# Kernel optimization log

Hardware: AMD Instinct MI355X
Metric: run time of the kernel (lower is better)

Reference implementation:

```python
import jax, jax.numpy as jnp
import numpy as np

B, L, D, H = 2, 2048, 1024, 16
DH = D // H


def setup_inputs() -> dict:
    key = jax.random.key(0)
    ks = jax.random.split(key, 5)
    bound = 1.0 / D ** 0.5
    x = jax.random.normal(ks[0], (B, L, D), dtype=jnp.float32)
    # causal mask: 0 means masked out
    mask = jnp.tril(jnp.ones((L, L), dtype=jnp.int32))[None].repeat(B, axis=0)
    Wq = jax.random.uniform(ks[1], (D, D), jnp.float32, -bound, bound)
    Wk = jax.random.uniform(ks[2], (D, D), jnp.float32, -bound, bound)
    Wv = jax.random.uniform(ks[3], (D, D), jnp.float32, -bound, bound)
    Wo = jax.random.uniform(ks[4], (D, D), jnp.float32, -bound, bound)
    return {"x": x, "mask": mask, "Wq": Wq, "Wk": Wk, "Wv": Wv, "Wo": Wo}


def _split_heads(t):
    # (B, L, D) -> (B, H, L, DH)
    b, l, _ = t.shape
    return t.reshape(b, l, H, DH).transpose(0, 2, 1, 3)


def reference(x, mask, Wq, Wk, Wv, Wo):
    # projections: torch Linear does x @ W.T with W:(out,in)
    q = _split_heads(x @ Wq.T)  # (B,H,L,DH)
    k = _split_heads(x @ Wk.T)
    v = _split_heads(x @ Wv.T)
    scores = jnp.einsum('bhqd,bhkd->bhqk', q, k) / jnp.sqrt(jnp.float32(DH))
    m = mask[:, None, :, :]  # (B,1,L,L)
    scores = jnp.where(m == 0, jnp.float32(-jnp.inf), scores)
    attn = jax.nn.softmax(scores, axis=-1)
    out = jnp.einsum('bhqk,bhkd->bhqd', attn, v)  # (B,H,L,DH)
    out = out.transpose(0, 2, 1, 3).reshape(x.shape[0], x.shape[1], D)
    return out @ Wo.T
```

## Files before the change

kernel.cpp:

```cpp
#include <hip/hip_runtime.h>
#include <stdint.h>


typedef unsigned short u16;
typedef __attribute__((ext_vector_type(8))) short short8;
typedef __attribute__((ext_vector_type(4))) float f32x4;
typedef __attribute__((ext_vector_type(4))) unsigned int uint4v;

#define NEG_BIG (-1e30f)
#define QSCALE 0.18033688011112042f

__device__ __forceinline__ f32x4 mfma16(short8 a, short8 b, f32x4 c) {
    return __builtin_amdgcn_mfma_f32_16x16x32_bf16(a, b, c, 0, 0, 0);
}

__device__ __forceinline__ u16 f2bf(float f) {
    uint32_t u = __float_as_uint(f);
    u += 0x7fffu + ((u >> 16) & 1u);
    return (u16)(u >> 16);
}

__device__ __forceinline__ float bf2f(u16 v) {
    return __uint_as_float((uint32_t)v << 16);
}

#if __has_builtin(__builtin_amdgcn_cvt_pk_bf16_f32)
__device__ __forceinline__ unsigned int f2bf_pk(float a, float b) {
    return __builtin_bit_cast(unsigned int, __builtin_amdgcn_cvt_pk_bf16_f32(a, b));
}
#else
__device__ __forceinline__ unsigned int f2bf_pk(float a, float b) {
    return (unsigned int)f2bf(a) | ((unsigned int)f2bf(b) << 16);
}
#endif

__device__ __forceinline__ void load_lds_16B(const u16* g, u16* lds_base) {
    __builtin_amdgcn_global_load_lds(
        (__attribute__((address_space(1))) void*)(uintptr_t)(const void*)g,
        (__attribute__((address_space(3))) void*)lds_base,
        16, 0, 0);
}

__global__ __launch_bounds__(256) void cvt_kernel(
    const float* __restrict__ x, const float* __restrict__ wq, const float* __restrict__ wk,
    const float* __restrict__ wv, const float* __restrict__ wo, u16* __restrict__ dst)
{
    const int gid = blockIdx.x * 256 + threadIdx.x;
    const float* src; size_t off;
    if (gid < 524288)      { src = x;  off = (size_t)gid * 8; }
    else if (gid < 655360) { src = wq; off = (size_t)(gid - 524288) * 8; }
    else if (gid < 786432) { src = wk; off = (size_t)(gid - 655360) * 8; }
    else if (gid < 917504) { src = wv; off = (size_t)(gid - 786432) * 8; }
    else                   { src = wo; off = (size_t)(gid - 917504) * 8; }
    float4 a = *(const float4*)(src + off);
    float4 b = *(const float4*)(src + off + 4);
    uint4v u = { f2bf_pk(a.x, a.y), f2bf_pk(a.z, a.w),
                 f2bf_pk(b.x, b.y), f2bf_pk(b.z, b.w) };
    *(uint4v*)(dst + (size_t)gid * 8) = u;
}

__device__ __forceinline__ void gemm_bt_128x128_bk64(
    const u16* __restrict__ A, const u16* __restrict__ Bw,
    u16* at, u16* bt, int m0, int n0, f32x4 acc[4][4])
{
    const int tid  = threadIdx.x;
    const int w    = tid >> 6, lane = tid & 63;
    const int quad = lane >> 4, l15 = lane & 15;
    const int wm   = (w >> 1) * 64, wn = (w & 1) * 64;
    const int srow = lane >> 3;
    const int sch  = lane & 7;

    for (int k0 = 0; k0 < 1024; k0 += 64) {
#pragma unroll
        for (int c = 0; c < 4; ++c) {
            int row = w * 32 + c * 8 + srow;
            int g   = sch ^ (row & 7);
            load_lds_16B(A  + (size_t)(m0 + row) * 1024 + k0 + g * 8, at + (w * 32 + c * 8) * 64);
            load_lds_16B(Bw + (size_t)(n0 + row) * 1024 + k0 + g * 8, bt + (w * 32 + c * 8) * 64);
        }
        __syncthreads();
#pragma unroll
        for (int ks = 0; ks < 2; ++ks) {
            short8 af[4], bf[4];
#pragma unroll
            for (int rf = 0; rf < 4; ++rf) {
                int ra = wm + rf * 16 + l15, pa = (ks * 4 + quad) ^ (ra & 7);
                af[rf] = *(const short8*)(at + ra * 64 + pa * 8);
                int rb = wn + rf * 16 + l15, pb = (ks * 4 + quad) ^ (rb & 7);
                bf[rf] = *(const short8*)(bt + rb * 64 + pb * 8);
            }
#pragma unroll
            for (int rf = 0; rf < 4; ++rf)
#pragma unroll
                for (int cf = 0; cf < 4; ++cf)
                    acc[rf][cf] = mfma16(af[rf], bf[cf], acc[rf][cf]);
        }
        __syncthreads();
    }
}

__global__ __launch_bounds__(256, 3) void qkv_gemm(
    const u16* __restrict__ xb, const u16* __restrict__ Wq, const u16* __restrict__ Wk,
    const u16* __restrict__ Wv, u16* __restrict__ qbuf, u16* __restrict__ kbuf,
    u16* __restrict__ vtbuf)
{
    __shared__ __align__(16) u16 at[128 * 64];
    __shared__ __align__(16) u16 bt[128 * 64];
    const int m0  = blockIdx.x * 128;
    const int by  = blockIdx.y;
    const int sel = by >> 3;
    const int n0  = (by & 7) * 128;
    const u16* Wsel = sel == 0 ? Wq : (sel == 1 ? Wk : Wv);

    f32x4 acc[4][4];
    const f32x4 z = {0.f, 0.f, 0.f, 0.f};
#pragma unroll
    for (int i = 0; i < 4; ++i)
#pragma unroll
        for (int j = 0; j < 4; ++j) acc[i][j] = z;

    gemm_bt_128x128_bk64(xb, Wsel, at, bt, m0, n0, acc);

    const int tid  = threadIdx.x, w = tid >> 6, lane = tid & 63;
    const int quad = lane >> 4, l15 = lane & 15;
    const int wm   = (w >> 1) * 64, wn = (w & 1) * 64;

    if (sel < 2) {
        u16* dst = sel == 0 ? qbuf : kbuf;
        const float scl = sel == 0 ? QSCALE : 1.0f;
#pragma unroll
        for (int rf = 0; rf < 4; ++rf)
#pragma unroll
            for (int cf = 0; cf < 4; ++cf) {
                int n = n0 + wn + cf * 16 + l15;
                int h = n >> 6, dh = n & 63;
#pragma unroll
                for (int r = 0; r < 4; ++r) {
                    int m = m0 + wm + rf * 16 + quad * 4 + r;
                    int b = m >> 11, l = m & 2047;
                    dst[(((size_t)(b * 16 + h)) * 2048 + l) * 64 + dh] = f2bf(acc[rf][cf][r] * scl);
                }
            }
    } else {
#pragma unroll
        for (int rf = 0; rf < 4; ++rf)
#pragma unroll
            for (int cf = 0; cf < 4; ++cf) {
                int n = n0 + wn + cf * 16 + l15;
                int h = n >> 6, dh = n & 63;
                int m = m0 + wm + rf * 16 + quad * 4;
                int b = m >> 11, l = m & 2047;
                ushort4 pk;
                pk.x = f2bf(acc[rf][cf][0]);
                pk.y = f2bf(acc[rf][cf][1]);
                pk.z = f2bf(acc[rf][cf][2]);
                pk.w = f2bf(acc[rf][cf][3]);
                *(ushort4*)(vtbuf + (((size_t)(b * 16 + h)) * 64 + dh) * 2048 + l) = pk;
            }
    }
}


struct Chain {
    short8 qf[2];
    f32x4  o[4];
    float  m, l;
};

__device__ __forceinline__ void attn_visit(
    const u16* ktb, const u16* vtb, u16* pw,
    Chain& c, int k0, int qrow, bool diag, int quad, int l15)
{
    const f32x4 z = {0.f, 0.f, 0.f, 0.f};
    f32x4 st[4];
#pragma unroll
    for (int nf = 0; nf < 4; ++nf) st[nf] = z;
#pragma unroll
    for (int ks = 0; ks < 2; ++ks)
#pragma unroll
        for (int nf = 0; nf < 4; ++nf) {
            int row = nf * 16 + l15;
            int ph  = (ks * 4 + quad) ^ (row & 7);
            short8 kf = *(const short8*)(ktb + row * 64 + ph * 8);
            st[nf] = mfma16(kf, c.qf[ks], st[nf]);
        }
    if (diag) {
#pragma unroll
        for (int nf = 0; nf < 4; ++nf)
#pragma unroll
            for (int r = 0; r < 4; ++r) {
                int key = k0 + nf * 16 + quad * 4 + r;
                if (key > qrow) st[nf][r] = NEG_BIG;
            }
    }
    {
        float mx = st[0][0];
#pragma unroll
        for (int nf = 0; nf < 4; ++nf)
#pragma unroll
            for (int r = 0; r < 4; ++r) mx = fmaxf(mx, st[nf][r]);
        mx = fmaxf(mx, __shfl_xor(mx, 16));
        mx = fmaxf(mx, __shfl_xor(mx, 32));
        float mnew = fmaxf(c.m, mx);
        float alpha = exp2f(c.m - mnew);
        float sum = 0.f;
#pragma unroll
        for (int nf = 0; nf < 4; ++nf)
#pragma unroll
            for (int r = 0; r < 4; ++r) {
                float p = exp2f(st[nf][r] - mnew);
                st[nf][r] = p;
                sum += p;
            }
        sum += __shfl_xor(sum, 16);
        sum += __shfl_xor(sum, 32);
        c.l = c.l * alpha + sum;
        c.m = mnew;
#pragma unroll
        for (int df = 0; df < 4; ++df) c.o[df] *= alpha;
    }
#pragma unroll
    for (int nf = 0; nf < 4; ++nf) {
        int ph = (nf * 2 + (quad >> 1)) ^ (l15 & 7);
        uint2 pk2;
        pk2.x = f2bf_pk(st[nf][0], st[nf][1]);
        pk2.y = f2bf_pk(st[nf][2], st[nf][3]);
        *(uint2*)(pw + l15 * 64 + ph * 8 + (quad & 1) * 4) = pk2;
    }
#pragma unroll
    for (int ks2 = 0; ks2 < 2; ++ks2) {
        int phb = (ks2 * 4 + quad) ^ (l15 & 7);
        short8 pb = *(const short8*)(pw + l15 * 64 + phb * 8);
#pragma unroll
        for (int df = 0; df < 4; ++df) {
            int row = df * 16 + l15;
            int ph  = (ks2 * 4 + quad) ^ (row & 7);
            short8 vf = *(const short8*)(vtb + row * 64 + ph * 8);
            c.o[df] = mfma16(vf, pb, c.o[df]);
        }
    }
}

__global__ __launch_bounds__(256, 4) void attn_kernel(
    const u16* __restrict__ qbuf, const u16* __restrict__ kbuf,
    const u16* __restrict__ vtbuf, u16* __restrict__ attn,
    u16* __restrict__ po, float* __restrict__ pm, float* __restrict__ pl)
{
    __shared__ __align__(16) u16 kt[2][64 * 64];
    __shared__ __align__(16) u16 vt[2][64 * 64];
    __shared__ __align__(16) u16 pt[4 * 16 * 64];

    const int tid  = threadIdx.x, w = tid >> 6, lane = tid & 63;
    const int quad = lane >> 4, l15 = lane & 15;
    const int bh   = blockIdx.y;
    const int a    = blockIdx.x >> 1;
    const int role = blockIdx.x & 1;
    const int jqS  = a, jqB = 31 - a;

    const u16* qbase = qbuf  + (size_t)bh * 2048 * 64;
    const u16* kbase = kbuf  + (size_t)bh * 2048 * 64;
    const u16* vbase = vtbuf + (size_t)bh * 64 * 2048;
    u16* pw = pt + w * (16 * 64);
    const int b = bh >> 4, h = bh & 15;
    const int rowi = w * 16 + l15;

    const f32x4 z = {0.f, 0.f, 0.f, 0.f};

    auto stage = [&](int t, int buf) {
        const int k0 = t * 64;
#pragma unroll
        for (int c = 0; c < 2; ++c) {
            int row = w * 16 + c * 8 + (lane >> 3);
            int g   = (lane & 7) ^ (row & 7);
            load_lds_16B(kbase + (size_t)(k0 + row) * 64 + g * 8, kt[buf] + (w * 16 + c * 8) * 64);
            load_lds_16B(vbase + (size_t)row * 2048 + k0 + g * 8, vt[buf] + (w * 16 + c * 8) * 64);
        }
    };

    auto load_q = [&](int jq, Chain& c) {
        int qw = jq * 64 + w * 16;
#pragma unroll
        for (int ks = 0; ks < 2; ++ks)
            c.qf[ks] = *(const short8*)(qbase + (size_t)(qw + l15) * 64 + ks * 32 + quad * 8);
        c.m = NEG_BIG; c.l = 0.f;
#pragma unroll
        for (int df = 0; df < 4; ++df) c.o[df] = z;
    };

    if (role == 0) {
        Chain cS, cB;
        load_q(jqS, cS);
        load_q(jqB, cB);
        const int tS = a, tB = 15 - a;
        const int T0 = tS > tB ? tS : tB;
        stage(0, 0);
        for (int t = 0; t <= T0; ++t) {
            __syncthreads();
            if (t < T0) stage(t + 1, (t + 1) & 1);
            const u16* ktb = kt[t & 1];
            const u16* vtb = vt[t & 1];
            const int k0 = t * 64;
            if (t <= tB) attn_visit(ktb, vtb, pw, cB, k0, 0, false, quad, l15);
            if (t <= tS) attn_visit(ktb, vtb, pw, cS, k0, jqS * 64 + rowi, t == tS, quad, l15);
        }
        {
            float inv = 1.f / cS.l;
            int qrow = jqS * 64 + rowi;
            u16* obase = attn + ((size_t)(b * 2048 + qrow)) * 1024 + h * 64;
#pragma unroll
            for (int df = 0; df < 4; ++df)
#pragma unroll
                for (int r = 0; r < 4; ++r)
                    obase[df * 16 + quad * 4 + r] = f2bf(cS.o[df][r] * inv);
        }
        {
            int p = (bh * 16 + a) * 2 + 0;
            u16* ob = po + (size_t)p * 4096 + rowi * 64;
#pragma unroll
            for (int df = 0; df < 4; ++df)
#pragma unroll
                for (int r = 0; r < 4; ++r)
                    ob[df * 16 + quad * 4 + r] = f2bf(cB.o[df][r]);
            if (quad == 0) { pm[p * 64 + rowi] = cB.m; pl[p * 64 + rowi] = cB.l; }
        }
    } else {
        Chain cB;
        load_q(jqB, cB);
        const int tb = 16 - a, te = 31 - a;
        stage(tb, tb & 1);
        for (int t = tb; t <= te; ++t) {
            __syncthreads();
            if (t < te) stage(t + 1, (t + 1) & 1);
            attn_visit(kt[t & 1], vt[t & 1], pw, cB, t * 64, jqB * 64 + rowi, t == te, quad, l15);
        }
        int p = (bh * 16 + a) * 2 + 1;
        u16* ob = po + (size_t)p * 4096 + rowi * 64;
#pragma unroll
        for (int df = 0; df < 4; ++df)
#pragma unroll
            for (int r = 0; r < 4; ++r)
                ob[df * 16 + quad * 4 + r] = f2bf(cB.o[df][r]);
        if (quad == 0) { pm[p * 64 + rowi] = cB.m; pl[p * 64 + rowi] = cB.l; }
    }
}

__global__ __launch_bounds__(256) void merge_kernel(
    const u16* __restrict__ po, const float* __restrict__ pm, const float* __restrict__ pl,
    u16* __restrict__ attn)
{
    const int u   = blockIdx.x;
    const int bh  = u >> 4, a = u & 15;
    const int b   = bh >> 4, h = bh & 15;
    const int jqB = 31 - a;
    const int row = threadIdx.x >> 2, seg = threadIdx.x & 3;
    const int p0  = u * 2, p1 = u * 2 + 1;

    float m0 = pm[p0 * 64 + row], m1 = pm[p1 * 64 + row];
    float l0 = pl[p0 * 64 + row], l1 = pl[p1 * 64 + row];
    float m  = fmaxf(m0, m1);
    float w0 = exp2f(m0 - m), w1 = exp2f(m1 - m);
    float inv = 1.f / (l0 * w0 + l1 * w1);
    w0 *= inv; w1 *= inv;

    const u16* o0p = po + (size_t)p0 * 4096 + row * 64 + seg * 16;
    const u16* o1p = po + (size_t)p1 * 4096 + row * 64 + seg * 16;
    short8 o0a = *(const short8*)(o0p);
    short8 o0b = *(const short8*)(o0p + 8);
    short8 o1a = *(const short8*)(o1p);
    short8 o1b = *(const short8*)(o1p + 8);

    float r[16];
#pragma unroll
    for (int j = 0; j < 8; ++j) {
        r[j]     = bf2f((u16)o0a[j]) * w0 + bf2f((u16)o1a[j]) * w1;
        r[8 + j] = bf2f((u16)o0b[j]) * w0 + bf2f((u16)o1b[j]) * w1;
    }
    uint4v pka = { f2bf_pk(r[0], r[1]), f2bf_pk(r[2], r[3]), f2bf_pk(r[4], r[5]), f2bf_pk(r[6], r[7]) };
    uint4v pkb = { f2bf_pk(r[8], r[9]), f2bf_pk(r[10], r[11]), f2bf_pk(r[12], r[13]), f2bf_pk(r[14], r[15]) };
    u16* dst = attn + ((size_t)(b * 2048 + jqB * 64 + row)) * 1024 + h * 64 + seg * 16;
    *(uint4v*)(dst)     = pka;
    *(uint4v*)(dst + 8) = pkb;
}

__global__ __launch_bounds__(256, 3) void oproj_gemm(
    const u16* __restrict__ attn, const u16* __restrict__ Wo, float* __restrict__ out)
{
    __shared__ __align__(16) u16 at[128 * 64];
    __shared__ __align__(16) u16 bt[64 * 64];
    const int m0 = blockIdx.x * 128;
    const int n0 = blockIdx.y * 64;

    const int tid  = threadIdx.x, w = tid >> 6, lane = tid & 63;
    const int quad = lane >> 4, l15 = lane & 15;
    const int wm   = (w >> 1) * 64, wn = (w & 1) * 32;
    const int srow = lane >> 3, sch = lane & 7;

    f32x4 acc[4][2];
    const f32x4 z = {0.f, 0.f, 0.f, 0.f};
#pragma unroll
    for (int i = 0; i < 4; ++i)
#pragma unroll
        for (int j = 0; j < 2; ++j) acc[i][j] = z;

    for (int k0 = 0; k0 < 1024; k0 += 64) {
#pragma unroll
        for (int c = 0; c < 4; ++c) {
            int row = w * 32 + c * 8 + srow;
            int g   = sch ^ (row & 7);
            load_lds_16B(attn + (size_t)(m0 + row) * 1024 + k0 + g * 8, at + (w * 32 + c * 8) * 64);
        }
#pragma unroll
        for (int c = 0; c < 2; ++c) {
            int row = w * 16 + c * 8 + srow;
            int g   = sch ^ (row & 7);
            load_lds_16B(Wo + (size_t)(n0 + row) * 1024 + k0 + g * 8, bt + (w * 16 + c * 8) * 64);
        }
        __syncthreads();
#pragma unroll
        for (int ks = 0; ks < 2; ++ks) {
            short8 af[4], bf[2];
#pragma unroll
            for (int rf = 0; rf < 4; ++rf) {
                int ra = wm + rf * 16 + l15, pa = (ks * 4 + quad) ^ (ra & 7);
                af[rf] = *(const short8*)(at + ra * 64 + pa * 8);
            }
#pragma unroll
            for (int cf = 0; cf < 2; ++cf) {
                int rb = wn + cf * 16 + l15, pb = (ks * 4 + quad) ^ (rb & 7);
                bf[cf] = *(const short8*)(bt + rb * 64 + pb * 8);
            }
#pragma unroll
            for (int rf = 0; rf < 4; ++rf)
#pragma unroll
                for (int cf = 0; cf < 2; ++cf)
                    acc[rf][cf] = mfma16(af[rf], bf[cf], acc[rf][cf]);
        }
        __syncthreads();
    }

#pragma unroll
    for (int rf = 0; rf < 4; ++rf)
#pragma unroll
        for (int cf = 0; cf < 2; ++cf) {
            int n = n0 + wn + cf * 16 + l15;
#pragma unroll
            for (int r = 0; r < 4; ++r) {
                int m = m0 + wm + rf * 16 + quad * 4 + r;
                out[(size_t)m * 1024 + n] = acc[rf][cf][r];
            }
        }
}

extern "C" void kernel_launch(void* const* d_in, const int* in_sizes, int n_in,
                              void* d_out, int out_size, void* d_ws, size_t ws_size,
                              hipStream_t stream) {
    const float* x  = (const float*)d_in[0];
    const float* Wq = (const float*)d_in[2];
    const float* Wk = (const float*)d_in[3];
    const float* Wv = (const float*)d_in[4];
    const float* Wo = (const float*)d_in[5];

    u16* ws    = (u16*)d_ws;
    const size_t M = 1024 * 1024;
    u16* qbuf  = ws;
    u16* kbuf  = ws + 4 * M;
    u16* vtb   = ws + 8 * M;
    u16* attnb = ws + 12 * M;
    u16* cvtb  = ws + 16 * M;
    u16* xb    = cvtb;
    u16* wqb   = cvtb + 4 * M;
    u16* wkb   = cvtb + 5 * M;
    u16* wvb   = cvtb + 6 * M;
    u16* wob   = cvtb + 7 * M;
    float* out = (float*)d_out;

    u16*   po = cvtb;
    float* pmv = (float*)(cvtb + 4 * M);
    float* plv = pmv + 32 * 16 * 2 * 64;

    cvt_kernel<<<4096, 256, 0, stream>>>(x, Wq, Wk, Wv, Wo, cvtb);
    qkv_gemm<<<dim3(32, 24), 256, 0, stream>>>(xb, wqb, wkb, wvb, qbuf, kbuf, vtb);
    attn_kernel<<<dim3(32, 32), 256, 0, stream>>>(qbuf, kbuf, vtb, attnb, po, pmv, plv);
    merge_kernel<<<512, 256, 0, stream>>>(po, pmv, plv, attnb);
    oproj_gemm<<<dim3(32, 16), 256, 0, stream>>>(attnb, wob, out);
}
```

Measured before the change: 205.9 us.

## Restructure attention inner loop with lazy rescale, MFMA row-sum, precomputed LDS addresses

Rewrites the flash-attention visit as a lambda with precomputed swizzled LDS pointers and incremental global staging pointers, so per-iteration address arithmetic goes away. The running max is only updated when a new score exceeds the stored max by more than a threshold, which skips most alpha rescaling. The softmax row sum now comes from an extra MFMA with a ones vector on the bf16 P tiles instead of shuffles, and s_setprio is raised around the MFMA bursts. The lazy rescale lets exponentials grow up to 2^8 before renormalising, and the row sum is taken from bf16-rounded probabilities, which changes numerics slightly.

After: 197.2 us. -4.2%, faster.

```diff
diff --git a/kernel.cpp b/kernel.cpp
--- a/kernel.cpp
+++ b/kernel.cpp
@@ -167,91 +167,16 @@
     float  m, l;
 };
 
-__device__ __forceinline__ void attn_visit(
-    const u16* ktb, const u16* vtb, u16* pw,
-    Chain& c, int k0, int qrow, bool diag, int quad, int l15)
-{
-    const f32x4 z = {0.f, 0.f, 0.f, 0.f};
-    f32x4 st[4];
-#pragma unroll
-    for (int nf = 0; nf < 4; ++nf) st[nf] = z;
-#pragma unroll
-    for (int ks = 0; ks < 2; ++ks)
-#pragma unroll
-        for (int nf = 0; nf < 4; ++nf) {
-            int row = nf * 16 + l15;
-            int ph  = (ks * 4 + quad) ^ (row & 7);
-            short8 kf = *(const short8*)(ktb + row * 64 + ph * 8);
-            st[nf] = mfma16(kf, c.qf[ks], st[nf]);
-        }
-    if (diag) {
-#pragma unroll
-        for (int nf = 0; nf < 4; ++nf)
-#pragma unroll
-            for (int r = 0; r < 4; ++r) {
-                int key = k0 + nf * 16 + quad * 4 + r;
-                if (key > qrow) st[nf][r] = NEG_BIG;
-            }
-    }
-    {
-        float mx = st[0][0];
-#pragma unroll
-        for (int nf = 0; nf < 4; ++nf)
-#pragma unroll
-            for (int r = 0; r < 4; ++r) mx = fmaxf(mx, st[nf][r]);
-        mx = fmaxf(mx, __shfl_xor(mx, 16));
-        mx = fmaxf(mx, __shfl_xor(mx, 32));
-        float mnew = fmaxf(c.m, mx);
-        float alpha = exp2f(c.m - mnew);
-        float sum = 0.f;
-#pragma unroll
-        for (int nf = 0; nf < 4; ++nf)
-#pragma unroll
-            for (int r = 0; r < 4; ++r) {
-                float p = exp2f(st[nf][r] - mnew);
-                st[nf][r] = p;
-                sum += p;
-            }
-        sum += __shfl_xor(sum, 16);
-        sum += __shfl_xor(sum, 32);
-        c.l = c.l * alpha + sum;
-        c.m = mnew;
-#pragma unroll
-        for (int df = 0; df < 4; ++df) c.o[df] *= alpha;
-    }
-#pragma unroll
-    for (int nf = 0; nf < 4; ++nf) {
-        int ph = (nf * 2 + (quad >> 1)) ^ (l15 & 7);
-        uint2 pk2;
-        pk2.x = f2bf_pk(st[nf][0], st[nf][1]);
-        pk2.y = f2bf_pk(st[nf][2], st[nf][3]);
-        *(uint2*)(pw + l15 * 64 + ph * 8 + (quad & 1) * 4) = pk2;
-    }
-#pragma unroll
-    for (int ks2 = 0; ks2 < 2; ++ks2) {
-        int phb = (ks2 * 4 + quad) ^ (l15 & 7);
-        short8 pb = *(const short8*)(pw + l15 * 64 + phb * 8);
-#pragma unroll
-        for (int df = 0; df < 4; ++df) {
-            int row = df * 16 + l15;
-            int ph  = (ks2 * 4 + quad) ^ (row & 7);
-            short8 vf = *(const short8*)(vtb + row * 64 + ph * 8);
-            c.o[df] = mfma16(vf, pb, c.o[df]);
-        }
-    }
-}
-
 __global__ __launch_bounds__(256, 4) void attn_kernel(
     const u16* __restrict__ qbuf, const u16* __restrict__ kbuf,
     const u16* __restrict__ vtbuf, u16* __restrict__ attn,
     u16* __restrict__ po, float* __restrict__ pm, float* __restrict__ pl)
 {
-    __shared__ __align__(16) u16 kt[2][64 * 64];
-    __shared__ __align__(16) u16 vt[2][64 * 64];
-    __shared__ __align__(16) u16 pt[4 * 16 * 64];
+    __shared__ __align__(16) u16 smem[20480];
 
     const int tid  = threadIdx.x, w = tid >> 6, lane = tid & 63;
     const int quad = lane >> 4, l15 = lane & 15;
+    const int e3   = l15 & 7;
     const int bh   = blockIdx.y;
     const int a    = blockIdx.x >> 1;
     const int role = blockIdx.x & 1;
@@ -260,21 +185,43 @@
     const u16* qbase = qbuf  + (size_t)bh * 2048 * 64;
     const u16* kbase = kbuf  + (size_t)bh * 2048 * 64;
     const u16* vbase = vtbuf + (size_t)bh * 64 * 2048;
-    u16* pw = pt + w * (16 * 64);
     const int b = bh >> 4, h = bh & 15;
     const int rowi = w * 16 + l15;
 
+    u16* const bk0 = smem + l15 * 64 + ((quad ^ e3) * 8);
+    u16* const bk1 = smem + l15 * 64 + (((4 + quad) ^ e3) * 8);
+    const u16* const pb0 = bk0 + 16384 + w * 1024;
+    const u16* const pb1 = bk1 + 16384 + w * 1024;
+    u16* pwp[4];
+#pragma unroll
+    for (int nf = 0; nf < 4; ++nf)
+        pwp[nf] = smem + 16384 + w * 1024 + l15 * 64
+                + (((nf * 2 + (quad >> 1)) ^ e3) * 8) + (quad & 1) * 4;
+
+    const int srow = w * 16 + (lane >> 3);
+    const int gofs = ((lane & 7) ^ (lane >> 3)) * 8;
+    const u16* kg0 = kbase + (size_t)srow * 64 + gofs;
+    const u16* kg1 = kg0 + 8 * 64;
+    const u16* vg0 = vbase + (size_t)srow * 2048 + gofs;
+    const u16* vg1 = vg0 + 8 * 2048;
+    u16* const kd0 = smem + w * 16 * 64;
+    u16* const kd1 = kd0 + 512;
+    u16* const vd0 = kd0 + 8192;
+    u16* const vd1 = kd1 + 8192;
+
+    short8 ones;
+#pragma unroll
+    for (int j = 0; j < 8; ++j) ones[j] = (short)0x3F80;
+
     const f32x4 z = {0.f, 0.f, 0.f, 0.f};
 
-    auto stage = [&](int t, int buf) {
-        const int k0 = t * 64;
-#pragma unroll
-        for (int c = 0; c < 2; ++c) {
-            int row = w * 16 + c * 8 + (lane >> 3);
-            int g   = (lane & 7) ^ (row & 7);
-            load_lds_16B(kbase + (size_t)(k0 + row) * 64 + g * 8, kt[buf] + (w * 16 + c * 8) * 64);
-            load_lds_16B(vbase + (size_t)row * 2048 + k0 + g * 8, vt[buf] + (w * 16 + c * 8) * 64);
-        }
+    auto stage = [&](int buf) {
+        const int bo = buf << 12;
+        load_lds_16B(kg0, kd0 + bo);
+        load_lds_16B(kg1, kd1 + bo);
+        load_lds_16B(vg0, vd0 + bo);
+        load_lds_16B(vg1, vd1 + bo);
+        kg0 += 4096; kg1 += 4096; vg0 += 64; vg1 += 64;
     };
 
     auto load_q = [&](int jq, Chain& c) {
@@ -285,6 +232,62 @@
         c.m = NEG_BIG; c.l = 0.f;
 #pragma unroll
         for (int df = 0; df < 4; ++df) c.o[df] = z;
+    };
+
+    auto visit = [&](const u16* c0, const u16* c1, Chain& c, int k0, int qrow, bool diag) {
+        f32x4 st[4] = {z, z, z, z};
+        __builtin_amdgcn_s_setprio(1);
+#pragma unroll
+        for (int nf = 0; nf < 4; ++nf)
+            st[nf] = mfma16(*(const short8*)(c0 + nf * 1024), c.qf[0], st[nf]);
+#pragma unroll
+        for (int nf = 0; nf < 4; ++nf)
+            st[nf] = mfma16(*(const short8*)(c1 + nf * 1024), c.qf[1], st[nf]);
+        __builtin_amdgcn_s_setprio(0);
+        if (diag) {
+            const int thr = qrow - k0 - quad * 4;
+#pragma unroll
+            for (int nf = 0; nf < 4; ++nf)
+#pragma unroll
+                for (int r = 0; r < 4; ++r)
+                    if (nf * 16 + r > thr) st[nf][r] = NEG_BIG;
+        }
+        float m0 = fmaxf(fmaxf(st[0][0], st[0][1]), fmaxf(st[0][2], st[0][3]));
+        float m1 = fmaxf(fmaxf(st[1][0], st[1][1]), fmaxf(st[1][2], st[1][3]));
+        float m2 = fmaxf(fmaxf(st[2][0], st[2][1]), fmaxf(st[2][2], st[2][3]));
+        float m3 = fmaxf(fmaxf(st[3][0], st[3][1]), fmaxf(st[3][2], st[3][3]));
+        float mx = fmaxf(fmaxf(m0, m1), fmaxf(m2, m3));
+        mx = fmaxf(mx, __shfl_xor(mx, 16));
+        mx = fmaxf(mx, __shfl_xor(mx, 32));
+        if (!__all(mx <= c.m + 8.0f)) {
+            float mnew = fmaxf(c.m, mx);
+            float alpha = exp2f(c.m - mnew);
+#pragma unroll
+            for (int df = 0; df < 4; ++df) c.o[df] *= alpha;
+            c.l *= alpha;
+            c.m = mnew;
+        }
+#pragma unroll
+        for (int nf = 0; nf < 4; ++nf) {
+            uint2 pk2;
+            pk2.x = f2bf_pk(exp2f(st[nf][0] - c.m), exp2f(st[nf][1] - c.m));
+            pk2.y = f2bf_pk(exp2f(st[nf][2] - c.m), exp2f(st[nf][3] - c.m));
+            *(uint2*)pwp[nf] = pk2;
+        }
+        short8 pv0 = *(const short8*)pb0;
+        short8 pv1 = *(const short8*)pb1;
+        f32x4 ls = z;
+        __builtin_amdgcn_s_setprio(1);
+        ls = mfma16(ones, pv0, ls);
+#pragma unroll
+        for (int df = 0; df < 4; ++df)
+            c.o[df] = mfma16(*(const short8*)(c0 + 8192 + df * 1024), pv0, c.o[df]);
+        ls = mfma16(ones, pv1, ls);
+#pragma unroll
+        for (int df = 0; df < 4; ++df)
+            c.o[df] = mfma16(*(const short8*)(c1 + 8192 + df * 1024), pv1, c.o[df]);
+        __builtin_amdgcn_s_setprio(0);
+        c.l += ls[0];
     };
 
     if (role == 0) {
@@ -293,15 +296,15 @@
         load_q(jqB, cB);
         const int tS = a, tB = 15 - a;
         const int T0 = tS > tB ? tS : tB;
-        stage(0, 0);
+        stage(0);
         for (int t = 0; t <= T0; ++t) {
             __syncthreads();
-            if (t < T0) stage(t + 1, (t + 1) & 1);
-            const u16* ktb = kt[t & 1];
-            const u16* vtb = vt[t & 1];
-            const int k0 = t * 64;
-            if (t <= tB) attn_visit(ktb, vtb, pw, cB, k0, 0, false, quad, l15);
-            if (t <= tS) attn_visit(ktb, vtb, pw, cS, k0, jqS * 64 + rowi, t == tS, quad, l15);
+            if (t < T0) stage((t + 1) & 1);
+            const int bo = (t & 1) << 12;
+            const u16* c0 = bk0 + bo;
+            const u16* c1 = bk1 + bo;
+            if (t <= tB) visit(c0, c1, cB, 0, 0, false);
+            if (t <= tS) visit(c0, c1, cS, t * 64, jqS * 64 + rowi, t == tS);
         }
         {
             float inv = 1.f / cS.l;
@@ -327,11 +330,14 @@
         Chain cB;
         load_q(jqB, cB);
         const int tb = 16 - a, te = 31 - a;
-        stage(tb, tb & 1);
+        kg0 += (size_t)tb * 4096; kg1 += (size_t)tb * 4096;
+        vg0 += tb * 64; vg1 += tb * 64;
+        stage(tb & 1);
         for (int t = tb; t <= te; ++t) {
             __syncthreads();
-            if (t < te) stage(t + 1, (t + 1) & 1);
-            attn_visit(kt[t & 1], vt[t & 1], pw, cB, t * 64, jqB * 64 + rowi, t == te, quad, l15);
+            if (t < te) stage((t + 1) & 1);
+            const int bo = (t & 1) << 12;
+            visit(bk0 + bo, bk1 + bo, cB, t * 64, jqB * 64 + rowi, t == te);
         }
         int p = (bh * 16 + a) * 2 + 1;
         u16* ob = po + (size_t)p * 4096 + rowi * 64;
```
